# Performance work log

Measured on AMD Instinct MI355X. Metric: run time of the kernel, lower is better.

## Reference

```python
import jax, jax.numpy as jnp
import numpy as np
from functools import partial

BETA_F = 1.0        # layer default beta_f
DOUBLING_ITERS = 21 # covers tree depth up to 2**21; random recursive tree depth ~ O(log N)


def setup_inputs() -> dict:
    key = jax.random.key(0)
    ks = jax.random.split(key, 6)
    N, K = 2_000_000, 8
    H, W = 2048, 2048
    attrs2d = jax.random.uniform(ks[0], (N, K), dtype=jnp.float32)  # normalized attrs in [a,1]
    weight = jax.random.normal(ks[1], (K,), dtype=jnp.float32)
    bias = jax.random.normal(ks[2], (1,), dtype=jnp.float32)
    levels = jax.random.uniform(ks[3], (N,), dtype=jnp.float32)
    # valid component tree: parent[i] < i for i>0, root = 0
    u = jax.random.uniform(ks[4], (N,))
    parent = jnp.floor(u * jnp.arange(N, dtype=jnp.float32)).astype(jnp.int32)
    pixel_node = jax.random.randint(ks[5], (H, W), 0, N, dtype=jnp.int32)
    return {"attrs2d": attrs2d, "weight": weight, "bias": bias,
            "levels": levels, "parent": parent, "pixel_node": pixel_node}


def _tree_filter(sigmoid, levels, parent, pixel_node):
    """Connected (direct-rule) filtering on a component tree.

    Each node contributes sigma(node) * (level(node) - level(parent));
    the filtered value of a pixel is the sum of contributions along the
    root-to-node path (root contributes its full level).
    Path sums are computed with pointer doubling (fully vectorized).
    """
    N = levels.shape[0]
    contrib = sigmoid * (levels - levels[parent])          # (N,)
    contrib = contrib.at[0].set(levels[0])                 # root keeps its level
    # sentinel node N with zero contribution, parent of root -> sentinel
    contrib_e = jnp.concatenate([contrib, jnp.zeros((1,), contrib.dtype)])
    par_e = jnp.concatenate([parent.at[0].set(N), jnp.array([N], jnp.int32)])

    def step(carry, _):
        s, p = carry
        return (s + s[p], p[p]), None

    (s, _), _ = jax.lax.scan(step, (contrib_e, par_e), None, length=DOUBLING_ITERS)
    y_nodes = s[:N]                                        # filtered gray value per node
    return y_nodes[pixel_node]                             # (H, W)


def reference(attrs2d, weight, bias, levels, parent, pixel_node):
    logits = attrs2d @ weight + bias[0]                    # (N,)
    s = BETA_F * logits                                    # clamp_logits=False (layer default)
    sigmoid = jax.nn.sigmoid(s)
    return _tree_filter(sigmoid, levels, parent, pixel_node)
```

## Files before the change

kernel.cpp:

```cpp
#include <hip/hip_runtime.h>
#include <hip/hip_fp16.h>

typedef float vf4 __attribute__((ext_vector_type(4)));
typedef int   vi4 __attribute__((ext_vector_type(4)));

struct SP { float s; int p; };

__device__ __forceinline__ SP ldSP(const SP* __restrict__ ptr) {
    float2 v = *reinterpret_cast<const float2*>(ptr);
    SP r; r.s = v.x; r.p = __float_as_int(v.y);
    return r;
}
__device__ __forceinline__ void stSP(SP* __restrict__ ptr, float s, int p) {
    float2 v; v.x = s; v.y = __int_as_float(p);
    *reinterpret_cast<float2*>(ptr) = v;
}

#define T_PREFIX 524288

__global__ void k_contrib(const float* __restrict__ attrs,
                          const float* __restrict__ weight,
                          const float* __restrict__ bias,
                          const float* __restrict__ levels,
                          const int*   __restrict__ parent,
                          SP* __restrict__ buf, int N) {
    float w0 = weight[0], w1 = weight[1], w2 = weight[2], w3 = weight[3];
    float w4 = weight[4], w5 = weight[5], w6 = weight[6], w7 = weight[7];
    float b = bias[0];
    int stride = gridDim.x * blockDim.x;
    const vf4* a4 = reinterpret_cast<const vf4*>(attrs);
    for (int i = blockIdx.x * blockDim.x + threadIdx.x; i < N; i += stride) {
        vf4 a0 = __builtin_nontemporal_load(&a4[2 * (size_t)i]);
        vf4 a1 = __builtin_nontemporal_load(&a4[2 * (size_t)i + 1]);
        float x = a0.x * w0 + a0.y * w1 + a0.z * w2 + a0.w * w3
                + a1.x * w4 + a1.y * w5 + a1.z * w6 + a1.w * w7 + b;
        float sg = 1.0f / (1.0f + __expf(-x));
        int p = parent[i];
        float c = sg * (levels[i] - levels[p]);
        if (i == 0) {
            stSP(&buf[0], levels[0], N);
        } else {
            stSP(&buf[i], c, p);
        }
    }
}

__global__ void k_prefix(const SP* __restrict__ buf,
                         float* __restrict__ yPre,
                         __half* __restrict__ y16, int T) {
    int i = blockIdx.x * blockDim.x + threadIdx.x;
    if (i >= T) return;
    float acc = 0.0f;
    int p = i;
    while (p < T) {
        SP w = ldSP(&buf[p]);
        acc += w.s;
        p = w.p;
    }
    yPre[i] = acc;
    y16[i] = __float2half(acc);
}

__global__ void k_chase(const SP* __restrict__ buf,
                        const float* __restrict__ yPre,
                        __half* __restrict__ y16, int T, int N) {
    int i = T + blockIdx.x * blockDim.x + threadIdx.x;
    if (i >= N) return;
    float acc = 0.0f;
    int p = i;
    while (p >= T) {
        SP w = ldSP(&buf[p]);
        acc += w.s;
        p = w.p;
    }
    y16[i] = __float2half(acc + yPre[p]);
}

__global__ void k_gather(const __half* __restrict__ y,
                         const int*   __restrict__ pix,
                         float*       __restrict__ out, int M) {
    int stride = gridDim.x * blockDim.x;
    int M4 = M >> 2;
    const vi4* pix4 = reinterpret_cast<const vi4*>(pix);
    vf4* out4 = reinterpret_cast<vf4*>(out);
    for (int i = blockIdx.x * blockDim.x + threadIdx.x; i < M4; i += stride) {
        vi4 p = __builtin_nontemporal_load(&pix4[i]);
        vf4 o;
        o.x = __half2float(y[p.x]);
        o.y = __half2float(y[p.y]);
        o.z = __half2float(y[p.z]);
        o.w = __half2float(y[p.w]);
        __builtin_nontemporal_store(o, &out4[i]);
    }
    int tid = blockIdx.x * blockDim.x + threadIdx.x;
    for (int i = (M4 << 2) + tid; i < M; i += stride) {
        out[i] = __half2float(y[pix[i]]);
    }
}

extern "C" void kernel_launch(void* const* d_in, const int* in_sizes, int n_in,
                              void* d_out, int out_size, void* d_ws, size_t ws_size,
                              hipStream_t stream) {
    const float* attrs  = (const float*)d_in[0];
    const float* weight = (const float*)d_in[1];
    const float* bias   = (const float*)d_in[2];
    const float* levels = (const float*)d_in[3];
    const int*   parent = (const int*)d_in[4];
    const int*   pix    = (const int*)d_in[5];
    float* out = (float*)d_out;

    const int N = in_sizes[3];
    const int M = out_size;
    const int T = T_PREFIX;

    SP* buf      = (SP*)d_ws;
    __half* y16  = (__half*)(buf + N);
    float* yPre  = (float*)(y16 + N);

    const int BLK = 256;

    k_contrib<<<2048, BLK, 0, stream>>>(attrs, weight, bias, levels, parent, buf, N);
    k_prefix <<<(T + BLK - 1) / BLK, BLK, 0, stream>>>(buf, yPre, y16, T);
    k_chase  <<<(N - T + BLK - 1) / BLK, BLK, 0, stream>>>(buf, yPre, y16, T, N);
    k_gather <<<2048, BLK, 0, stream>>>(y16, pix, out, M);
}
```

Baseline: 104.1 us.

## Split tree path-sum into four index-range levels with chained prefix reuse

Replaces the two-stage prefix/chase scheme with a single generic kernel launched over four increasing node-index ranges. Each range walks parent pointers only until it falls below its lower bound, then adds the already-computed full path sum stored for that ancestor. This shortens the pointer-chasing chains, especially in the prefix region, in exchange for two extra kernel launches and a larger fp32 result array.

```diff
diff --git a/kernel.cpp b/kernel.cpp
--- a/kernel.cpp
+++ b/kernel.cpp
@@ -15,8 +15,6 @@
     float2 v; v.x = s; v.y = __int_as_float(p);
     *reinterpret_cast<float2*>(ptr) = v;
 }
-
-#define T_PREFIX 524288
 
 __global__ void k_contrib(const float* __restrict__ attrs,
                           const float* __restrict__ weight,
@@ -45,35 +43,22 @@
     }
 }
 
-__global__ void k_prefix(const SP* __restrict__ buf,
-                         float* __restrict__ yPre,
-                         __half* __restrict__ y16, int T) {
-    int i = blockIdx.x * blockDim.x + threadIdx.x;
-    if (i >= T) return;
+__global__ void k_level(const SP* __restrict__ buf,
+                        float* __restrict__ yAll,
+                        __half* __restrict__ y16,
+                        int lo, int hi, int N) {
+    int i = lo + blockIdx.x * blockDim.x + threadIdx.x;
+    if (i >= hi) return;
     float acc = 0.0f;
     int p = i;
-    while (p < T) {
+    while (p >= lo && p < N) {
         SP w = ldSP(&buf[p]);
         acc += w.s;
         p = w.p;
     }
-    yPre[i] = acc;
+    if (p < lo) acc += yAll[p];
+    yAll[i] = acc;
     y16[i] = __float2half(acc);
-}
-
-__global__ void k_chase(const SP* __restrict__ buf,
-                        const float* __restrict__ yPre,
-                        __half* __restrict__ y16, int T, int N) {
-    int i = T + blockIdx.x * blockDim.x + threadIdx.x;
-    if (i >= N) return;
-    float acc = 0.0f;
-    int p = i;
-    while (p >= T) {
-        SP w = ldSP(&buf[p]);
-        acc += w.s;
-        p = w.p;
-    }
-    y16[i] = __float2half(acc + yPre[p]);
 }
 
 __global__ void k_gather(const __half* __restrict__ y,
@@ -111,16 +96,20 @@
 
     const int N = in_sizes[3];
     const int M = out_size;
-    const int T = T_PREFIX;
 
     SP* buf      = (SP*)d_ws;
     __half* y16  = (__half*)(buf + N);
-    float* yPre  = (float*)(y16 + N);
+    float* yAll  = (float*)(y16 + N);
 
     const int BLK = 256;
 
     k_contrib<<<2048, BLK, 0, stream>>>(attrs, weight, bias, levels, parent, buf, N);
-    k_prefix <<<(T + BLK - 1) / BLK, BLK, 0, stream>>>(buf, yPre, y16, T);
-    k_chase  <<<(N - T + BLK - 1) / BLK, BLK, 0, stream>>>(buf, yPre, y16, T, N);
-    k_gather <<<2048, BLK, 0, stream>>>(y16, pix, out, M);
+
+    const int T0 = 0, T1 = 32768, T2 = 131072, T3 = 524288;
+    k_level<<<(T1 - T0 + BLK - 1) / BLK, BLK, 0, stream>>>(buf, yAll, y16, T0, T1, N);
+    k_level<<<(T2 - T1 + BLK - 1) / BLK, BLK, 0, stream>>>(buf, yAll, y16, T1, T2, N);
+    k_level<<<(T3 - T2 + BLK - 1) / BLK, BLK, 0, stream>>>(buf, yAll, y16, T2, T3, N);
+    k_level<<<(N  - T3 + BLK - 1) / BLK, BLK, 0, stream>>>(buf, yAll, y16, T3, N,  N);
+
+    k_gather<<<2048, BLK, 0, stream>>>(y16, pix, out, M);
 }
```

Result: no change. 102.1 us (-1.9%).
